# Kernel optimization log

Measured on AMD Instinct MI355X. Metric: run time of the kernel, lower is better.

## Reference

```python
import jax, jax.numpy as jnp
import numpy as np

VOCAB, EMB, HID = 32000, 512, 1024


def setup_inputs() -> dict:
    key = jax.random.key(0)
    k1, k2, k3, k4, k5, k6 = jax.random.split(key, 6)
    sentences = jax.random.randint(k1, (64, 512), 0, VOCAB)
    emb_table = jax.random.normal(k2, (VOCAB, EMB), dtype=jnp.float32)
    s_ih = 1.0 / np.sqrt(HID)
    # PyTorch LSTM params: gate order (i, f, g, o)
    w_ih = jax.random.uniform(k3, (4 * HID, EMB), minval=-s_ih, maxval=s_ih, dtype=jnp.float32)
    w_hh = jax.random.uniform(k4, (4 * HID, HID), minval=-s_ih, maxval=s_ih, dtype=jnp.float32)
    b_ih = jax.random.uniform(k5, (4 * HID,), minval=-s_ih, maxval=s_ih, dtype=jnp.float32)
    b_hh = jax.random.uniform(k6, (4 * HID,), minval=-s_ih, maxval=s_ih, dtype=jnp.float32)
    return {"sentences": sentences, "emb_table": emb_table,
            "w_ih": w_ih, "w_hh": w_hh, "b_ih": b_ih, "b_hh": b_hh}


def _lstm_forward(emb_table, w_ih, w_hh, b_ih, b_hh, sentences):
    B = sentences.shape[0]
    H = w_hh.shape[1]
    # embedding lookup -> [T, B, E] (matches transpose(0,1) in torch code)
    embedded = emb_table[sentences].transpose(1, 0, 2)
    # precompute input projections for all timesteps: [T, B, 4H]
    x_gates = jnp.einsum('tbe,ge->tbg', embedded, w_ih) + b_ih + b_hh

    def step(carry, xg):
        h, c = carry
        gates = xg + h @ w_hh.T  # [B, 4H]
        i, f, g, o = jnp.split(gates, 4, axis=-1)
        i = jax.nn.sigmoid(i)
        f = jax.nn.sigmoid(f)
        g = jnp.tanh(g)
        o = jax.nn.sigmoid(o)
        c_new = f * c + i * g
        h_new = o * jnp.tanh(c_new)
        return (h_new, c_new), None

    h0 = jnp.zeros((B, H), dtype=emb_table.dtype)
    c0 = jnp.zeros((B, H), dtype=emb_table.dtype)
    (h, c), _ = jax.lax.scan(step, (h0, c0), x_gates)
    # original returns output of last step only: [1, B, H], and (h, c) each [1, B, H]
    return h[None], (h[None], c[None])


def reference(sentences, emb_table, w_ih, w_hh, b_ih, b_hh):
    output, (h, c) = _lstm_forward(emb_table, w_ih, w_hh, b_ih, b_hh, sentences)
    return output, h, c
```

## Files before the change

kernel.cpp:

```cpp
#include <hip/hip_runtime.h>

typedef __bf16 bf16x8 __attribute__((ext_vector_type(8)));
typedef float f32x4 __attribute__((ext_vector_type(4)));
typedef unsigned short u16;
typedef unsigned long long u64;

#define NSTEP 512

#define AL(p)   __hip_atomic_load((p), __ATOMIC_RELAXED, __HIP_MEMORY_SCOPE_AGENT)
#define AS(p,v) __hip_atomic_store((p), (v), __ATOMIC_RELAXED, __HIP_MEMORY_SCOPE_AGENT)

__device__ __forceinline__ u16 f2bf(float f) {
  union { float f; unsigned u; } x; x.f = f;
  return (u16)((x.u + 0x7fffu + ((x.u >> 16) & 1u)) >> 16);
}

__global__ void prep_kernel(u64* __restrict__ H0, int* __restrict__ F) {
  int i = blockIdx.x * blockDim.x + threadIdx.x;
  if (i < 16384) AS(H0 + i, 0ULL);
  if (i < 32768) AS(&F[i], 0);
}

__global__ void gather_kernel(const int* __restrict__ sent, const float* __restrict__ emb,
                              u16* __restrict__ A1) {
  int row = blockIdx.x * 4 + (threadIdx.x >> 6);
  int lane = threadIdx.x & 63;
  int t = row >> 6, b = row & 63;
  int idx = sent[b * 512 + t];
  const float* src = emb + (size_t)idx * 512 + lane * 8;
  u16* dst = A1 + (size_t)row * 512 + lane * 8;
  #pragma unroll
  for (int k = 0; k < 8; ++k) dst[k] = f2bf(src[k]);
}

__global__ void __launch_bounds__(256, 2)
lstm_kernel(const u16* __restrict__ A1,
            const float* __restrict__ wih, const float* __restrict__ whh,
            const float* __restrict__ bih, const float* __restrict__ bhh,
            u16* __restrict__ H, float* __restrict__ out, int* __restrict__ F) {
  __shared__ u16 wlds[48 * 16 * 36];
  __shared__ alignas(8) u16 hx[4][16][4];

  const int j   = blockIdx.x;
  const int tid = threadIdx.x;
  const int w   = tid >> 6;
  const int l   = tid & 63;
  const int lr  = l & 15, lk = l >> 4;
  const int g   = lr >> 2, nn = lr & 3;
  const int wrow = g * 1024 + j * 4 + nn;

  for (int task = tid; task < 3072; task += 256) {
    int kk = task >> 6;
    int rem = task & 63;
    int rb = rem >> 2, q = rem & 3;
    int row = (rb >> 2) * 1024 + j * 4 + (rb & 3);
    const float* src = (kk < 16) ? (wih + (size_t)row * 512 + kk * 32 + q * 8)
                                 : (whh + (size_t)row * 1024 + (kk - 16) * 32 + q * 8);
    u16* dst = wlds + (kk * 16 + rb) * 36 + q * 8;
    #pragma unroll
    for (int e = 0; e < 8; ++e) dst[e] = f2bf(src[e]);
  }
  __syncthreads();

  const float bias = bih[wrow] + bhh[wrow];
  const float sca = (g == 2) ? 2.f : 1.f;
  const float bd  = (g == 2) ? -1.f : 0.f;
  const int arow = w * 16 + lr;
  const u16* bx = wlds + lr * 36 + lk * 8;

  float cst[4] = {0.f, 0.f, 0.f, 0.f};

  bf16x8 ax[16];
  {
    const u16* apre = A1 + (size_t)arow * 512 + lk * 8;
    #pragma unroll
    for (int kk = 0; kk < 16; ++kk) ax[kk] = *(const bf16x8*)(apre + kk * 32);
  }

  union AF { bf16x8 v; u64 q[2]; };

#define FADDR(c) (F + (((c) * 64 + l) * 128) + w * 32)
#define WAITV(vv, c)                                                        \
  { while (vv < t) { __builtin_amdgcn_s_sleep(1); vv = AL(FADDR(c)); } }
#define LD8(BUF, CH)                                                        \
  { _Pragma("unroll")                                                       \
    for (int r = 0; r < 8; ++r)                                             \
      BUF[r].v = *(const bf16x8*)(hp + (CH) * 256 + r * 32); }
#define MM8(ACC, BUF, W0)                                                   \
  { _Pragma("unroll")                                                       \
    for (int r = 0; r < 8; ++r) {                                           \
      bf16x8 b = *(const bf16x8*)(bx + ((W0) + r) * 576);                   \
      ACC = __builtin_amdgcn_mfma_f32_16x16x32_bf16(BUF[r].v, b, ACC, 0, 0, 0); \
    } }

  #pragma unroll 1
  for (int t = 0; t < NSTEP; ++t) {
    AF ha[8], hb[8];
    const u16* hp = H + (size_t)t * 65536 + (size_t)arow * 1024 + lk * 8;
    int v0 = AL(FADDR(0));
    int v1 = AL(FADDR(1));
    int v2 = AL(FADDR(2));
    int v3 = AL(FADDR(3));
    f32x4 acx = { bias, bias, bias, bias };
    #pragma unroll
    for (int kk = 0; kk < 8; ++kk) {
      bf16x8 b = *(const bf16x8*)(bx + kk * 576);
      acx = __builtin_amdgcn_mfma_f32_16x16x32_bf16(ax[kk], b, acx, 0, 0, 0);
    }
    WAITV(v0, 0);
    LD8(ha, 0);
    WAITV(v1, 1);
    LD8(hb, 1);
    #pragma unroll
    for (int kk = 8; kk < 16; ++kk) {
      bf16x8 b = *(const bf16x8*)(bx + kk * 576);
      acx = __builtin_amdgcn_mfma_f32_16x16x32_bf16(ax[kk], b, acx, 0, 0, 0);
    }
    f32x4 ac1 = { 0.f, 0.f, 0.f, 0.f };
    f32x4 ac2 = { 0.f, 0.f, 0.f, 0.f };
    MM8(ac1, ha, 16);
    WAITV(v2, 2);
    LD8(ha, 2);
    MM8(ac2, hb, 24);
    WAITV(v3, 3);
    LD8(hb, 3);
    MM8(ac1, ha, 32);
    MM8(ac2, hb, 40);

    float hv4[4], cn4[4];
    #pragma unroll
    for (int r = 0; r < 4; ++r) {
      float xv = acx[r] + ac1[r] + ac2[r];
      float act = sca / (1.f + __expf(-sca * xv)) + bd;
      float gg = __shfl_xor(act, 8);
      float ff = __shfl_xor(act, 4);
      float oo = __shfl_xor(act, 12);
      float cn = ff * cst[r] + act * gg;
      cst[r] = cn;
      float tc = 2.f / (1.f + __expf(-2.f * cn)) - 1.f;
      hv4[r] = oo * tc;
      cn4[r] = cn;
    }

    if (t == NSTEP - 1) {
      if (lr < 4) {
        #pragma unroll
        for (int r = 0; r < 4; ++r) {
          int R = w * 16 + lk * 4 + r;
          out[(size_t)R * 1024 + j * 4 + lr]          = hv4[r];
          out[65536 + (size_t)R * 1024 + j * 4 + lr]  = hv4[r];
          out[131072 + (size_t)R * 1024 + j * 4 + lr] = cn4[r];
        }
      }
    } else {
      if (lr < 4) {
        #pragma unroll
        for (int r = 0; r < 4; ++r) hx[w][lk * 4 + r][lr] = f2bf(hv4[r]);
      }
      if (l < 16) {
        u64 pk = *(const u64*)(&hx[w][l][0]);
        u16* hw = H + (size_t)(t + 1) * 65536 + (size_t)(w * 16 + l) * 1024 + j * 4;
        AS((u64*)hw, pk);
      }
      asm volatile("s_waitcnt vmcnt(0)" ::: "memory");
      if (l == 0) AS(F + j * 128 + w * 32, t + 1);
      {
        const u16* apre = A1 + ((size_t)(t + 1) * 64 + arow) * 512 + lk * 8;
        #pragma unroll
        for (int kk = 0; kk < 16; ++kk) ax[kk] = *(const bf16x8*)(apre + kk * 32);
      }
    }
  }
#undef FADDR
#undef WAITV
#undef LD8
#undef MM8
}

extern "C" void kernel_launch(void* const* d_in, const int* in_sizes, int n_in,
                              void* d_out, int out_size, void* d_ws, size_t ws_size,
                              hipStream_t stream) {
  const int*   sent = (const int*)d_in[0];
  const float* emb  = (const float*)d_in[1];
  const float* w_ih = (const float*)d_in[2];
  const float* w_hh = (const float*)d_in[3];
  const float* b_ih = (const float*)d_in[4];
  const float* b_hh = (const float*)d_in[5];
  float* out = (float*)d_out;

  char* ws = (char*)d_ws;
  u16* A1 = (u16*)ws;
  u16* H  = (u16*)(ws + 33554432);
  int* F  = (int*)(ws + 33554432 + 67108864);

  prep_kernel<<<256, 256, 0, stream>>>((u64*)H, F);
  gather_kernel<<<8192, 256, 0, stream>>>(sent, emb, A1);

  void* args[] = { (void*)&A1, (void*)&w_ih, (void*)&w_hh,
                   (void*)&b_ih, (void*)&b_hh, (void*)&H, (void*)&out, (void*)&F };
  hipError_t err = hipLaunchCooperativeKernel((void*)lstm_kernel, dim3(256), dim3(256),
                                              args, 0, stream);
  if (err != hipSuccess) {
    lstm_kernel<<<dim3(256), dim3(256), 0, stream>>>(A1, w_ih, w_hh, b_ih, b_hh,
                                                     H, out, F);
  }
}
```

Baseline: 4.237 ms.

## Use one per-block flag and wave-0 polling with LDS broadcast for step sync

Each block now publishes a single readiness flag per timestep after a __syncthreads, replacing one flag per wave. Only wave 0 polls global flags and relays readiness to the other waves through shared memory. This cuts global atomic polling traffic by a factor of four, but adds a block-wide barrier per step and an extra hop through LDS, which may add latency on the critical serial path.

```diff
diff --git a/kernel.cpp b/kernel.cpp
--- a/kernel.cpp
+++ b/kernel.cpp
@@ -18,7 +18,7 @@
 __global__ void prep_kernel(u64* __restrict__ H0, int* __restrict__ F) {
   int i = blockIdx.x * blockDim.x + threadIdx.x;
   if (i < 16384) AS(H0 + i, 0ULL);
-  if (i < 32768) AS(&F[i], 0);
+  if (i < 8192) AS(&F[i], 0);
 }
 
 __global__ void gather_kernel(const int* __restrict__ sent, const float* __restrict__ emb,
@@ -40,6 +40,7 @@
             u16* __restrict__ H, float* __restrict__ out, int* __restrict__ F) {
   __shared__ u16 wlds[48 * 16 * 36];
   __shared__ alignas(8) u16 hx[4][16][4];
+  __shared__ int ready[4];
 
   const int j   = blockIdx.x;
   const int tid = threadIdx.x;
@@ -48,6 +49,8 @@
   const int lr  = l & 15, lk = l >> 4;
   const int g   = lr >> 2, nn = lr & 3;
   const int wrow = g * 1024 + j * 4 + nn;
+
+  if (tid < 4) ready[tid] = 0;
 
   for (int task = tid; task < 3072; task += 256) {
     int kk = task >> 6;
@@ -79,9 +82,15 @@
 
   union AF { bf16x8 v; u64 q[2]; };
 
-#define FADDR(c) (F + (((c) * 64 + l) * 128) + w * 32)
-#define WAITV(vv, c)                                                        \
-  { while (vv < t) { __builtin_amdgcn_s_sleep(1); vv = AL(FADDR(c)); } }
+#define WAITC(c)                                                            \
+  { if (w == 0) {                                                           \
+      const int* fp = F + ((c) * 64 + l) * 32;                              \
+      int vv = AL(fp);                                                      \
+      while (vv < t) { __builtin_amdgcn_s_sleep(1); vv = AL(fp); }          \
+      if (l == 0) *(volatile int*)&ready[c] = t;                            \
+    } else {                                                                \
+      while (*(volatile int*)&ready[c] < t) __builtin_amdgcn_s_sleep(1);    \
+    } }
 #define LD8(BUF, CH)                                                        \
   { _Pragma("unroll")                                                       \
     for (int r = 0; r < 8; ++r)                                             \
@@ -97,19 +106,15 @@
   for (int t = 0; t < NSTEP; ++t) {
     AF ha[8], hb[8];
     const u16* hp = H + (size_t)t * 65536 + (size_t)arow * 1024 + lk * 8;
-    int v0 = AL(FADDR(0));
-    int v1 = AL(FADDR(1));
-    int v2 = AL(FADDR(2));
-    int v3 = AL(FADDR(3));
     f32x4 acx = { bias, bias, bias, bias };
     #pragma unroll
     for (int kk = 0; kk < 8; ++kk) {
       bf16x8 b = *(const bf16x8*)(bx + kk * 576);
       acx = __builtin_amdgcn_mfma_f32_16x16x32_bf16(ax[kk], b, acx, 0, 0, 0);
     }
-    WAITV(v0, 0);
+    WAITC(0);
     LD8(ha, 0);
-    WAITV(v1, 1);
+    WAITC(1);
     LD8(hb, 1);
     #pragma unroll
     for (int kk = 8; kk < 16; ++kk) {
@@ -119,10 +124,10 @@
     f32x4 ac1 = { 0.f, 0.f, 0.f, 0.f };
     f32x4 ac2 = { 0.f, 0.f, 0.f, 0.f };
     MM8(ac1, ha, 16);
-    WAITV(v2, 2);
+    WAITC(2);
     LD8(ha, 2);
     MM8(ac2, hb, 24);
-    WAITV(v3, 3);
+    WAITC(3);
     LD8(hb, 3);
     MM8(ac1, ha, 32);
     MM8(ac2, hb, 40);
@@ -163,7 +168,8 @@
         AS((u64*)hw, pk);
       }
       asm volatile("s_waitcnt vmcnt(0)" ::: "memory");
-      if (l == 0) AS(F + j * 128 + w * 32, t + 1);
+      __syncthreads();
+      if (tid == 0) AS(F + j * 32, t + 1);
       {
         const u16* apre = A1 + ((size_t)(t + 1) * 64 + arow) * 512 + lk * 8;
         #pragma unroll
@@ -171,8 +177,7 @@
       }
     }
   }
-#undef FADDR
-#undef WAITV
+#undef WAITC
 #undef LD8
 #undef MM8
 }
```

Measured after the change: 4.695 ms. 10.8% more time.

## Replace per-step flag polling with timestep-tagged hidden-state words

Applied to the files above, without the earlier changes.

Adds a new LSTM kernel that packs each pair of bf16 hidden values together with a 32-bit timestep tag into one 64-bit word. Consumers validate the tag on the data itself and retry, which removes the separate flag array, the store-then-flag ordering (vmcnt wait), and the flag polling round trip on every step. The cost is doubled hidden-state storage (128MB), a prep kernel that zeros all of it, and extra load bandwidth for the tags. The input-projection loads are no longer prefetched, and occupancy is set to 1 block per CU. The old path is kept as a fallback when the workspace is too small.

```diff
diff --git a/kernel.cpp b/kernel.cpp
--- a/kernel.cpp
+++ b/kernel.cpp
@@ -3,6 +3,7 @@
 typedef __bf16 bf16x8 __attribute__((ext_vector_type(8)));
 typedef float f32x4 __attribute__((ext_vector_type(4)));
 typedef unsigned short u16;
+typedef unsigned u32;
 typedef unsigned long long u64;
 
 #define NSTEP 512
@@ -15,7 +16,13 @@
   return (u16)((x.u + 0x7fffu + ((x.u >> 16) & 1u)) >> 16);
 }
 
-__global__ void prep_kernel(u64* __restrict__ H0, int* __restrict__ F) {
+__global__ void prepA_kernel(u64* __restrict__ H64) {
+  size_t i = (size_t)blockIdx.x * blockDim.x + threadIdx.x;
+  size_t stride = (size_t)gridDim.x * blockDim.x;
+  for (size_t k = i; k < (size_t)NSTEP * 32768; k += stride) H64[k] = 0;
+}
+
+__global__ void prepB_kernel(u64* __restrict__ H0, int* __restrict__ F) {
   int i = blockIdx.x * blockDim.x + threadIdx.x;
   if (i < 16384) AS(H0 + i, 0ULL);
   if (i < 32768) AS(&F[i], 0);
@@ -33,11 +40,155 @@
   for (int k = 0; k < 8; ++k) dst[k] = f2bf(src[k]);
 }
 
+__global__ void __launch_bounds__(256, 1)
+lstm_tag_kernel(const u16* __restrict__ A1,
+                const float* __restrict__ wih, const float* __restrict__ whh,
+                const float* __restrict__ bih, const float* __restrict__ bhh,
+                u64* __restrict__ H64, float* __restrict__ out) {
+  __shared__ u16 wlds[48 * 16 * 36];
+
+  const int j   = blockIdx.x;
+  const int tid = threadIdx.x;
+  const int w   = tid >> 6;
+  const int l   = tid & 63;
+  const int lr  = l & 15, lk = l >> 4;
+  const int g   = lr >> 2, nn = lr & 3;
+  const int wrow = g * 1024 + j * 4 + nn;
+
+  for (int task = tid; task < 3072; task += 256) {
+    int kk = task >> 6;
+    int rem = task & 63;
+    int rb = rem >> 2, q = rem & 3;
+    int row = (rb >> 2) * 1024 + j * 4 + (rb & 3);
+    const float* src = (kk < 16) ? (wih + (size_t)row * 512 + kk * 32 + q * 8)
+                                 : (whh + (size_t)row * 1024 + (kk - 16) * 32 + q * 8);
+    u16* dst = wlds + (kk * 16 + rb) * 36 + q * 8;
+    #pragma unroll
+    for (int e = 0; e < 8; ++e) dst[e] = f2bf(src[e]);
+  }
+  __syncthreads();
+
+  const float bias = bih[wrow] + bhh[wrow];
+  const float sca = (g == 2) ? 2.f : 1.f;
+  const float bd  = (g == 2) ? -1.f : 0.f;
+  const int arow = w * 16 + lr;
+  const u16* bx = wlds + lr * 36 + lk * 8;
+
+  float cst[4] = {0.f, 0.f, 0.f, 0.f};
+
+  union AF { bf16x8 v; u32 d[4]; };
+
+#define LD8C(BUF, BAD, CH)                                                  \
+  { BAD = 0;                                                                \
+    _Pragma("unroll")                                                       \
+    for (int r = 0; r < 8; ++r) {                                           \
+      const u64* p = hp64 + ((CH) * 8 + r) * 16 + lk * 4;                   \
+      u64 w0 = p[0], w1 = p[1], w2 = p[2], w3 = p[3];                       \
+      BUF[r].d[0] = (u32)w0; BUF[r].d[1] = (u32)w1;                         \
+      BUF[r].d[2] = (u32)w2; BUF[r].d[3] = (u32)w3;                         \
+      BAD |= ((u32)(w0 >> 32) ^ tu) | ((u32)(w1 >> 32) ^ tu)                \
+           | ((u32)(w2 >> 32) ^ tu) | ((u32)(w3 >> 32) ^ tu);               \
+    } }
+#define RTY(BUF, BAD, CH)                                                   \
+  while (BAD) {                                                             \
+    __builtin_amdgcn_s_sleep(2);                                            \
+    BAD = 0;                                                                \
+    _Pragma("unroll")                                                       \
+    for (int r = 0; r < 8; ++r) {                                           \
+      const u64* p = hp64 + ((CH) * 8 + r) * 16 + lk * 4;                   \
+      u64 w0 = AL(p), w1 = AL(p + 1), w2 = AL(p + 2), w3 = AL(p + 3);       \
+      BUF[r].d[0] = (u32)w0; BUF[r].d[1] = (u32)w1;                         \
+      BUF[r].d[2] = (u32)w2; BUF[r].d[3] = (u32)w3;                         \
+      BAD |= ((u32)(w0 >> 32) ^ tu) | ((u32)(w1 >> 32) ^ tu)                \
+           | ((u32)(w2 >> 32) ^ tu) | ((u32)(w3 >> 32) ^ tu);               \
+    } }
+#define MM8T(ACC, BUF, W0)                                                  \
+  { _Pragma("unroll")                                                       \
+    for (int r = 0; r < 8; ++r) {                                           \
+      bf16x8 b = *(const bf16x8*)(bx + ((W0) + r) * 576);                   \
+      ACC = __builtin_amdgcn_mfma_f32_16x16x32_bf16(BUF[r].v, b, ACC, 0, 0, 0); \
+    } }
+
+  #pragma unroll 1
+  for (int t = 0; t < NSTEP; ++t) {
+    const u32 tu = (u32)t;
+    const u64* hp64 = H64 + (size_t)t * 32768 + (size_t)arow * 512;
+    f32x4 acx = { bias, bias, bias, bias };
+    {
+      const u16* ap = A1 + ((size_t)t * 64 + arow) * 512 + lk * 8;
+      #pragma unroll
+      for (int kk = 0; kk < 16; ++kk) {
+        bf16x8 a = *(const bf16x8*)(ap + kk * 32);
+        bf16x8 b = *(const bf16x8*)(bx + kk * 576);
+        acx = __builtin_amdgcn_mfma_f32_16x16x32_bf16(a, b, acx, 0, 0, 0);
+      }
+    }
+    AF ha[8], hb[8], hc[8];
+    u32 bad0, bad1, bad2, bad3;
+    f32x4 ac1 = { 0.f, 0.f, 0.f, 0.f };
+    f32x4 ac2 = { 0.f, 0.f, 0.f, 0.f };
+    LD8C(ha, bad0, 0);
+    LD8C(hb, bad1, 1);
+    LD8C(hc, bad2, 2);
+    RTY(ha, bad0, 0);
+    MM8T(ac1, ha, 16);
+    LD8C(ha, bad3, 3);
+    RTY(hb, bad1, 1);
+    MM8T(ac2, hb, 24);
+    RTY(hc, bad2, 2);
+    MM8T(ac1, hc, 32);
+    RTY(ha, bad3, 3);
+    MM8T(ac2, ha, 40);
+
+    float hv4[4], cn4[4];
+    #pragma unroll
+    for (int r = 0; r < 4; ++r) {
+      float xv = acx[r] + ac1[r] + ac2[r];
+      float act = sca / (1.f + __expf(-sca * xv)) + bd;
+      float gg = __shfl_xor(act, 8);
+      float ff = __shfl_xor(act, 4);
+      float oo = __shfl_xor(act, 12);
+      float cn = ff * cst[r] + act * gg;
+      cst[r] = cn;
+      float tc = 2.f / (1.f + __expf(-2.f * cn)) - 1.f;
+      hv4[r] = oo * tc;
+      cn4[r] = cn;
+    }
+
+    if (t == NSTEP - 1) {
+      if (lr < 4) {
+        #pragma unroll
+        for (int r = 0; r < 4; ++r) {
+          int R = w * 16 + lk * 4 + r;
+          out[(size_t)R * 1024 + j * 4 + lr]          = hv4[r];
+          out[65536 + (size_t)R * 1024 + j * 4 + lr]  = hv4[r];
+          out[131072 + (size_t)R * 1024 + j * 4 + lr] = cn4[r];
+        }
+      }
+    } else {
+      const u32 tag = (u32)(t + 1);
+      u64* Hn = H64 + (size_t)(t + 1) * 32768;
+      #pragma unroll
+      for (int r = 0; r < 4; ++r) {
+        float hpart = __shfl_xor(hv4[r], 1);
+        if (lr < 4 && !(lr & 1)) {
+          int R = w * 16 + lk * 4 + r;
+          u64 pk = ((u64)tag << 32) | ((u32)f2bf(hpart) << 16) | (u32)f2bf(hv4[r]);
+          AS(Hn + (size_t)R * 512 + j * 2 + (lr >> 1), pk);
+        }
+      }
+    }
+  }
+#undef LD8C
+#undef RTY
+#undef MM8T
+}
+
 __global__ void __launch_bounds__(256, 2)
-lstm_kernel(const u16* __restrict__ A1,
-            const float* __restrict__ wih, const float* __restrict__ whh,
-            const float* __restrict__ bih, const float* __restrict__ bhh,
-            u16* __restrict__ H, float* __restrict__ out, int* __restrict__ F) {
+lstm_fb_kernel(const u16* __restrict__ A1,
+               const float* __restrict__ wih, const float* __restrict__ whh,
+               const float* __restrict__ bih, const float* __restrict__ bhh,
+               u16* __restrict__ H, float* __restrict__ out, int* __restrict__ F) {
   __shared__ u16 wlds[48 * 16 * 36];
   __shared__ alignas(8) u16 hx[4][16][4];
 
@@ -190,18 +341,32 @@
 
   char* ws = (char*)d_ws;
   u16* A1 = (u16*)ws;
-  u16* H  = (u16*)(ws + 33554432);
-  int* F  = (int*)(ws + 33554432 + 67108864);
-
-  prep_kernel<<<256, 256, 0, stream>>>((u64*)H, F);
+
+  const size_t needA = 33554432ull + 134217728ull;
+  const int tagged = (ws_size >= needA) ? 1 : 0;
+
   gather_kernel<<<8192, 256, 0, stream>>>(sent, emb, A1);
 
-  void* args[] = { (void*)&A1, (void*)&w_ih, (void*)&w_hh,
-                   (void*)&b_ih, (void*)&b_hh, (void*)&H, (void*)&out, (void*)&F };
-  hipError_t err = hipLaunchCooperativeKernel((void*)lstm_kernel, dim3(256), dim3(256),
-                                              args, 0, stream);
-  if (err != hipSuccess) {
-    lstm_kernel<<<dim3(256), dim3(256), 0, stream>>>(A1, w_ih, w_hh, b_ih, b_hh,
-                                                     H, out, F);
-  }
-}
+  if (tagged) {
+    u64* H64 = (u64*)(ws + 33554432);
+    prepA_kernel<<<4096, 256, 0, stream>>>(H64);
+    void* args[] = { (void*)&A1, (void*)&w_ih, (void*)&w_hh,
+                     (void*)&b_ih, (void*)&b_hh, (void*)&H64, (void*)&out };
+    hipError_t err = hipLaunchCooperativeKernel((void*)lstm_tag_kernel,
+                                                dim3(256), dim3(256), args, 0, stream);
+    if (err != hipSuccess)
+      lstm_tag_kernel<<<dim3(256), dim3(256), 0, stream>>>(A1, w_ih, w_hh,
+                                                           b_ih, b_hh, H64, out);
+  } else {
+    u16* H = (u16*)(ws + 33554432);
+    int* F = (int*)(ws + 33554432 + 67108864);
+    prepB_kernel<<<256, 256, 0, stream>>>((u64*)H, F);
+    void* args[] = { (void*)&A1, (void*)&w_ih, (void*)&w_hh,
+                     (void*)&b_ih, (void*)&b_hh, (void*)&H, (void*)&out, (void*)&F };
+    hipError_t err = hipLaunchCooperativeKernel((void*)lstm_fb_kernel,
+                                                dim3(256), dim3(256), args, 0, stream);
+    if (err != hipSuccess)
+      lstm_fb_kernel<<<dim3(256), dim3(256), 0, stream>>>(A1, w_ih, w_hh,
+                                                          b_ih, b_hh, H, out, F);
+  }
+}
```

Result: slower. 9.532 ms (+125.0%).
